# Kernel tuning notes

Hardware: AMD Instinct MI355X
Metric: run time of the kernel (lower is better)

## Reference

```python
import jax, jax.numpy as jnp
import numpy as np

N, E, G = 4096, 65536, 64
C_IN, PE_DIM, H, L, HEADS, C_OUT = 64, 24, 128, 2, 4, 10
HD = H // HEADS


def setup_inputs() -> dict:
    key = jax.random.key(0)
    ks = iter(jax.random.split(key, 64))

    def nrm(shape, scale=0.05):
        return jax.random.normal(next(ks), shape, jnp.float32) * scale

    inp = {}
    inp["x"] = jax.random.normal(next(ks), (N, C_IN), jnp.float32)
    inp["lap_pe"] = jax.random.normal(next(ks), (N, 8), jnp.float32)
    inp["rw_pe"] = jax.random.normal(next(ks), (N, 16), jnp.float32)
    inp["edge_index"] = jax.random.randint(next(ks), (2, E), 0, N)
    inp["batch"] = jnp.sort(jax.random.randint(next(ks), (N,), 0, G))
    inp["Wp"] = nrm((C_IN + PE_DIM, H)); inp["bp"] = jnp.zeros((H,), jnp.float32)
    inp["gin_W1"] = nrm((L, H, H)); inp["gin_b1"] = jnp.zeros((L, H), jnp.float32)
    inp["gin_W2"] = nrm((L, H, H)); inp["gin_b2"] = jnp.zeros((L, H), jnp.float32)
    inp["bn1_g"] = jnp.ones((L, H), jnp.float32); inp["bn1_b"] = jnp.zeros((L, H), jnp.float32)
    inp["bn2_g"] = jnp.ones((L, H), jnp.float32); inp["bn2_b"] = jnp.zeros((L, H), jnp.float32)
    inp["bn3_g"] = jnp.ones((L, H), jnp.float32); inp["bn3_b"] = jnp.zeros((L, H), jnp.float32)
    inp["attn_in_w"] = nrm((L, H, 3 * H)); inp["attn_in_b"] = jnp.zeros((L, 3 * H), jnp.float32)
    inp["attn_out_w"] = nrm((L, H, H)); inp["attn_out_b"] = jnp.zeros((L, H), jnp.float32)
    inp["mlp_W1"] = nrm((L, H, 2 * H)); inp["mlp_b1"] = jnp.zeros((L, 2 * H), jnp.float32)
    inp["mlp_W2"] = nrm((L, 2 * H, H)); inp["mlp_b2"] = jnp.zeros((L, H), jnp.float32)
    inp["Wr1"] = nrm((H, H)); inp["br1"] = jnp.zeros((H,), jnp.float32)
    inp["Wr2"] = nrm((H, H)); inp["br2"] = jnp.zeros((H,), jnp.float32)
    inp["Wc"] = nrm((H, C_OUT)); inp["bc"] = jnp.zeros((C_OUT,), jnp.float32)
    return inp


def _bn(x, g, b):
    # BatchNorm1d over node dim, training-mode batch statistics (biased var)
    m = jnp.mean(x, axis=0)
    v = jnp.var(x, axis=0)
    return (x - m) * jax.lax.rsqrt(v + 1e-5) * g + b


def reference(x, lap_pe, rw_pe, edge_index, batch, Wp, bp,
              gin_W1, gin_b1, gin_W2, gin_b2,
              bn1_g, bn1_b, bn2_g, bn2_b, bn3_g, bn3_b,
              attn_in_w, attn_in_b, attn_out_w, attn_out_b,
              mlp_W1, mlp_b1, mlp_W2, mlp_b2,
              Wr1, br1, Wr2, br2, Wc, bc):
    pe = jnp.concatenate([lap_pe, rw_pe], axis=-1)          # [N, 24]
    h = jnp.concatenate([x, pe], axis=-1) @ Wp + bp         # [N, H]
    src, dst = edge_index[0], edge_index[1]
    scale = 1.0 / np.sqrt(HD)
    for l in range(L):
        # --- local GINConv: (1+eps)*x_i + sum_{j->i} x_j, eps=0, then 2-layer MLP ---
        agg = jax.ops.segment_sum(h[src], dst, num_segments=N)
        g = h + agg
        g = jax.nn.relu(g @ gin_W1[l] + gin_b1[l]) @ gin_W2[l] + gin_b2[l]
        g = _bn(g + h, bn1_g[l], bn1_b[l])                  # residual + norm1
        # --- global MHA; batch is NOT forwarded to GPSConv, so all N nodes form one dense graph ---
        qkv = h @ attn_in_w[l] + attn_in_b[l]               # [N, 3H]
        q, k, v = jnp.split(qkv, 3, axis=-1)
        q = q.reshape(N, HEADS, HD).transpose(1, 0, 2)      # [Hh, N, d]
        k = k.reshape(N, HEADS, HD).transpose(1, 0, 2)
        v = v.reshape(N, HEADS, HD).transpose(1, 0, 2)
        a = jax.nn.softmax(jnp.einsum('hnd,hmd->hnm', q, k) * scale, axis=-1)
        o = jnp.einsum('hnm,hmd->hnd', a, v).transpose(1, 0, 2).reshape(N, H)
        o = o @ attn_out_w[l] + attn_out_b[l]
        o = _bn(o + h, bn2_g[l], bn2_b[l])                  # residual + norm2
        # --- combine + FFN (channels -> 2*channels -> channels) + norm3 ---
        out = g + o
        m = jax.nn.relu(out @ mlp_W1[l] + mlp_b1[l]) @ mlp_W2[l] + mlp_b2[l]
        out = _bn(out + m, bn3_g[l], bn3_b[l])
        h = jax.nn.relu(out)                                # outer F.relu in GraphGPS
    pooled = jax.ops.segment_sum(h, batch, num_segments=G)  # global_add_pool
    r = jax.nn.relu(pooled @ Wr1 + br1)
    r = jax.nn.relu(r @ Wr2 + br2)                          # dropout(0.5) disabled (eval)
    return r @ Wc + bc                                      # [G, C_OUT]
```

## Files before the change

kernel.cpp:

```cpp
#include <hip/hip_runtime.h>
#include <hip/hip_bf16.h>
#include <math.h>

#define NN 4096
#define HH 128
#define EE 65536
#define GG 64
#define KSPLIT 8
#define KLEN (NN / KSPLIT)
#define SMEM_BYTES 14336

typedef unsigned short u16;
typedef unsigned int u32;
typedef __bf16 bf16x8 __attribute__((ext_vector_type(8)));
typedef float f32x4 __attribute__((ext_vector_type(4)));

__device__ inline u16 f2b(float f) {
  u32 u = __float_as_uint(f);
  u += 0x7FFFu + ((u >> 16) & 1u);
  return (u16)(u >> 16);
}
__device__ inline u32 pkbf2(float a, float b) {
  __hip_bfloat162 h = __float22bfloat162_rn(float2{a, b});
  u32 u; __builtin_memcpy(&u, &h, 4); return u;
}

struct TDesc { const float* src; int Ks, K, M, off; };
struct TPack { TDesc d[13]; };

__global__ __launch_bounds__(256) void transcount_k(TPack P, u16* __restrict__ dst,
    const int* __restrict__ ei, int* cnt) {
  if (blockIdx.x >= 1344) {
    int e = (blockIdx.x - 1344)*256 + threadIdx.x;
    atomicAdd(&cnt[ei[EE + e]], 1);
    return;
  }
  int idx = blockIdx.x * 256 + threadIdx.x;
  for (int i = 0; i < 13; i++) {
    int sz = P.d[i].K * P.d[i].M;
    if (idx < sz) {
      int m = idx / P.d[i].K;
      int k = idx - m * P.d[i].K;
      float v = (k < P.d[i].Ks) ? P.d[i].src[(size_t)k * P.d[i].M + m] : 0.f;
      dst[P.d[i].off + idx] = f2b(v);
      return;
    }
    idx -= sz;
  }
}

__global__ __launch_bounds__(256) void scan_k(const int* __restrict__ cnt,
    int* __restrict__ rowptr, int* __restrict__ cursor) {
  __shared__ int tot[256];
  int t = threadIdx.x;
  int base = t * 16;
  int loc[16]; int s = 0;
  #pragma unroll
  for (int i = 0; i < 16; i++) { loc[i] = s; s += cnt[base + i]; }
  tot[t] = s;
  __syncthreads();
  for (int off = 1; off < 256; off <<= 1) {
    int v = (t >= off) ? tot[t - off] : 0;
    __syncthreads();
    tot[t] += v;
    __syncthreads();
  }
  int excl = (t == 0) ? 0 : tot[t - 1];
  #pragma unroll
  for (int i = 0; i < 16; i++) {
    int p = excl + loc[i];
    rowptr[base + i] = p; cursor[base + i] = p;
  }
  if (t == 255) rowptr[NN] = excl + s;
}

__global__ __launch_bounds__(256) void aggcsr_k(const int* __restrict__ rowptr,
    const int* __restrict__ elist, const float* __restrict__ h,
    float* __restrict__ agg) {
  int d = blockIdx.x*2 + (threadIdx.x >> 7);
  int c = threadIdx.x & 127;
  int beg = rowptr[d], end = rowptr[d + 1];
  float acc = 0.f;
  for (int j = beg; j < end; j++)
    acc += h[(size_t)elist[j]*HH + c];
  agg[(size_t)d*HH + c] = acc;
}

struct GArgs {
  const float *A, *A2, *A3;
  const u16* Bt;
  const float* bias;
  float* C;
  const float *res, *res2;
  float* stats;
  const float *sbase, *pg1, *pb1, *pg2, *pb2;
  const float *opart, *lpart;
  u16 *qb, *kb, *vt;
  int K, M;
};

template <int ASTAGE, int EPI, int RELU>
__device__ void mgemm_dev(const GArgs& a, int bx, int by, char* smem) {
  char* Ab = smem;
  char* Bb = smem + 4096;
  float* affs = (float*)(smem + 12288);
  const int tid = threadIdx.x;
  const int n0 = bx * 32, m0 = by * 64;
  const int w = tid >> 6, lane = tid & 63;
  const int g = lane >> 4, li = lane & 15;
  const int wr = w >> 1, wc = w & 1;
  const int K = a.K, M = a.M;

  if (ASTAGE == 2) {
    int plane = tid >> 7, cc = tid & 127;
    const float* st = a.sbase + plane*256;
    const float* gg = plane ? a.pg2 : a.pg1;
    const float* bb = plane ? a.pb2 : a.pb1;
    float mean = st[cc] * (1.f/NN);
    float var  = st[128+cc] * (1.f/NN) - mean*mean;
    float s = rsqrtf(var + 1e-5f) * gg[cc];
    affs[plane*256 + cc]       = s;
    affs[plane*256 + 128 + cc] = bb[cc] - mean*s;
    __syncthreads();
  }

  f32x4 acc0 = {0,0,0,0}, acc1 = {0,0,0,0};
  const int arow = tid >> 3, akseg = (tid & 7) * 8;
  const int bcol = tid >> 2, bkseg = (tid & 3) * 16;

  for (int k0 = 0; k0 < K; k0 += 64) {
    {
      float4 a0 = {0,0,0,0}, a1 = {0,0,0,0};
      if (ASTAGE == 4) {
        int n = n0 + arow;
        if (k0 == 0) {
          a0 = *(const float4*)&a.A[(size_t)n*64 + akseg];
          a1 = *(const float4*)&a.A[(size_t)n*64 + akseg + 4];
        } else {
          if (akseg == 0)       { a0 = *(const float4*)&a.A2[(size_t)n*8];
                                  a1 = *(const float4*)&a.A2[(size_t)n*8 + 4]; }
          else if (akseg == 8)  { a0 = *(const float4*)&a.A3[(size_t)n*16];
                                  a1 = *(const float4*)&a.A3[(size_t)n*16 + 4]; }
          else if (akseg == 16) { a0 = *(const float4*)&a.A3[(size_t)n*16 + 8];
                                  a1 = *(const float4*)&a.A3[(size_t)n*16 + 12]; }
        }
      } else if (ASTAGE == 3) {
        int n = n0 + arow, c = k0 + akseg;
        int head = c >> 5, d0 = c & 31;
        float4 o0 = {0,0,0,0}, o1 = {0,0,0,0}; float L = 0.f;
        #pragma unroll
        for (int s = 0; s < KSPLIT; s++) {
          const float* ob = a.opart + ((size_t)(s*4+head)*NN + n)*32 + d0;
          float4 x0 = *(const float4*)ob, x1 = *(const float4*)(ob + 4);
          o0.x += x0.x; o0.y += x0.y; o0.z += x0.z; o0.w += x0.w;
          o1.x += x1.x; o1.y += x1.y; o1.z += x1.z; o1.w += x1.w;
          L += a.lpart[(size_t)(s*4+head)*NN + n];
        }
        float inv = 1.f / L;
        a0 = make_float4(o0.x*inv, o0.y*inv, o0.z*inv, o0.w*inv);
        a1 = make_float4(o1.x*inv, o1.y*inv, o1.z*inv, o1.w*inv);
      } else {
        const float* ap = a.A + (size_t)(n0 + arow) * K + k0 + akseg;
        a0 = *(const float4*)ap; a1 = *(const float4*)(ap + 4);
        if (ASTAGE == 1) {
          const float* p2 = a.A2 + (size_t)(n0 + arow) * K + k0 + akseg;
          float4 c0 = *(const float4*)p2, c1 = *(const float4*)(p2 + 4);
          a0.x += c0.x; a0.y += c0.y; a0.z += c0.z; a0.w += c0.w;
          a1.x += c1.x; a1.y += c1.y; a1.z += c1.z; a1.w += c1.w;
        } else if (ASTAGE == 2) {
          const float* p2 = a.A2 + (size_t)(n0 + arow) * K + k0 + akseg;
          float4 c0 = *(const float4*)p2, c1 = *(const float4*)(p2 + 4);
          const float* af = affs + k0 + akseg;
          float4 s1a = *(const float4*)af,         s1b = *(const float4*)(af + 4);
          float4 t1a = *(const float4*)(af + 128), t1b = *(const float4*)(af + 132);
          float4 s2a = *(const float4*)(af + 256), s2b = *(const float4*)(af + 260);
          float4 t2a = *(const float4*)(af + 384), t2b = *(const float4*)(af + 388);
          a0.x = a0.x*s1a.x + t1a.x + c0.x*s2a.x + t2a.x;
          a0.y = a0.y*s1a.y + t1a.y + c0.y*s2a.y + t2a.y;
          a0.z = a0.z*s1a.z + t1a.z + c0.z*s2a.z + t2a.z;
          a0.w = a0.w*s1a.w + t1a.w + c0.w*s2a.w + t2a.w;
          a1.x = a1.x*s1b.x + t1b.x + c1.x*s2b.x + t2b.x;
          a1.y = a1.y*s1b.y + t1b.y + c1.y*s2b.y + t2b.y;
          a1.z = a1.z*s1b.z + t1b.z + c1.z*s2b.z + t2b.z;
          a1.w = a1.w*s1b.w + t1b.w + c1.w*s2b.w + t2b.w;
        }
      }
      u16 t8[8] = {f2b(a0.x), f2b(a0.y), f2b(a0.z), f2b(a0.w),
                   f2b(a1.x), f2b(a1.y), f2b(a1.z), f2b(a1.w)};
      *(uint4*)(Ab + ((arow*128 + akseg*2) ^ ((arow & 7) << 4))) = *(uint4*)t8;
    }
    {
      const u16* bp = a.Bt + (size_t)(m0 + bcol) * K + k0 + bkseg;
      uint4 b0 = *(const uint4*)bp;
      uint4 b1 = *(const uint4*)(bp + 8);
      int ba = bcol*128 + bkseg*2;
      int sw = (bcol & 7) << 4;
      *(uint4*)(Bb + (ba ^ sw)) = b0;
      *(uint4*)(Bb + ((ba + 16) ^ sw)) = b1;
    }
    __syncthreads();
    int row = wr*16 + li;
    int cAl = wc*32 + li, cBl = cAl + 16;
    #pragma unroll
    for (int ck = 0; ck < 2; ck++) {
      bf16x8 af = *(const bf16x8*)(Ab + ((row*128 + ck*64 + g*16) ^ ((row & 7) << 4)));
      bf16x8 bf0 = *(const bf16x8*)(Bb + ((cAl*128 + ck*64 + g*16) ^ ((cAl & 7) << 4)));
      bf16x8 bf1 = *(const bf16x8*)(Bb + ((cBl*128 + ck*64 + g*16) ^ ((cBl & 7) << 4)));
      acc0 = __builtin_amdgcn_mfma_f32_16x16x32_bf16(af, bf0, acc0, 0, 0, 0);
      acc1 = __builtin_amdgcn_mfma_f32_16x16x32_bf16(af, bf1, acc1, 0, 0, 0);
    }
    __syncthreads();
  }

  const int colA = m0 + wc*32 + li, colB = colA + 16;
  const int colAl = wc*32 + li, colBl = colAl + 16;
  const int rbase = n0 + wr*16 + 4*g;

  if (EPI == 0) {
    float b0 = a.bias[colA], b1 = a.bias[colB];
    #pragma unroll
    for (int r = 0; r < 4; r++) {
      float v0 = acc0[r] + b0, v1 = acc1[r] + b1;
      if (RELU) { v0 = fmaxf(v0, 0.f); v1 = fmaxf(v1, 0.f); }
      a.C[(size_t)(rbase + r) * M + colA] = v0;
      a.C[(size_t)(rbase + r) * M + colB] = v1;
    }
  } else if (EPI == 1 || EPI == 3) {
    float b0 = a.bias[colA], b1 = a.bias[colB];
    float sA1=0, tA1=0, sA2=0, tA2=0, sB1=0, tB1=0, sB2=0, tB2=0;
    if (EPI == 3) {
      auto mk = [&](int col, float& s1, float& t1, float& s2, float& t2) {
        float m1 = a.sbase[col]*(1.f/NN), v1 = a.sbase[128+col]*(1.f/NN) - m1*m1;
        s1 = rsqrtf(v1 + 1e-5f) * a.pg1[col]; t1 = a.pb1[col] - m1*s1;
        float m2 = a.sbase[256+col]*(1.f/NN), v2 = a.sbase[384+col]*(1.f/NN) - m2*m2;
        s2 = rsqrtf(v2 + 1e-5f) * a.pg2[col]; t2 = a.pb2[col] - m2*s2;
      };
      mk(colA, sA1, tA1, sA2, tA2);
      mk(colB, sB1, tB1, sB2, tB2);
    }
    float s0 = 0, q0 = 0, s1 = 0, q1 = 0;
    #pragma unroll
    for (int r = 0; r < 4; r++) {
      int rw2 = rbase + r;
      float v0, v1;
      if (EPI == 1) {
        v0 = acc0[r] + b0 + a.res[(size_t)rw2 * 128 + colA];
        v1 = acc1[r] + b1 + a.res[(size_t)rw2 * 128 + colB];
      } else {
        v0 = acc0[r] + b0 + a.res[(size_t)rw2*128 + colA]*sA1 + tA1
                          + a.res2[(size_t)rw2*128 + colA]*sA2 + tA2;
        v1 = acc1[r] + b1 + a.res[(size_t)rw2*128 + colB]*sB1 + tB1
                          + a.res2[(size_t)rw2*128 + colB]*sB2 + tB2;
      }
      a.C[(size_t)rw2 * M + colA] = v0;
      a.C[(size_t)rw2 * M + colB] = v1;
      s0 += v0; q0 += v0*v0; s1 += v1; q1 += v1*v1;
    }
    s0 += __shfl_xor(s0, 16); s0 += __shfl_xor(s0, 32);
    q0 += __shfl_xor(q0, 16); q0 += __shfl_xor(q0, 32);
    s1 += __shfl_xor(s1, 16); s1 += __shfl_xor(s1, 32);
    q1 += __shfl_xor(q1, 16); q1 += __shfl_xor(q1, 32);
    float* sred = (float*)smem;
    if (lane < 16) {
      sred[wr*64 + colAl] = s0;  sred[128 + wr*64 + colAl] = q0;
      sred[wr*64 + colBl] = s1;  sred[128 + wr*64 + colBl] = q1;
    }
    __syncthreads();
    if (tid < 128) {
      int c = tid & 63, isq = tid >> 6;
      float v = sred[isq*128 + c] + sred[isq*128 + 64 + c];
      atomicAdd(&a.stats[isq*128 + m0 + c], v);
    }
  } else {
    const float QS = 0.17677669529663687f * 1.4426950408889634f;
    auto doq = [&](int col, f32x4 acc, float bb) {
      if (col < 128) {
        int hd = col >> 5, d = col & 31;
        #pragma unroll
        for (int r = 0; r < 4; r++)
          a.qb[((size_t)hd*NN + rbase + r)*32 + d] = f2b((acc[r] + bb) * QS);
      } else if (col < 256) {
        int hd = (col - 128) >> 5, d = col & 31;
        #pragma unroll
        for (int r = 0; r < 4; r++)
          a.kb[((size_t)hd*NN + rbase + r)*32 + d] = f2b(acc[r] + bb);
      } else {
        #pragma unroll
        for (int r = 0; r < 4; r++)
          a.vt[(size_t)(col - 256)*NN + rbase + r] = f2b(acc[r] + bb);
      }
    };
    doq(colA, acc0, a.bias[colA]);
    doq(colB, acc1, a.bias[colB]);
  }
}

template <int AS, int EP, int RE>
__global__ __launch_bounds__(256) void k_gemm(GArgs a) {
  extern __shared__ char smem[];
  mgemm_dev<AS, EP, RE>(a, blockIdx.x, blockIdx.y, smem);
}

__global__ __launch_bounds__(256) void k_qkv_gin1(GArgs qa, GArgs ga) {
  extern __shared__ char smem[];
  int b = blockIdx.x;
  if (b < 768) mgemm_dev<0,4,0>(qa, b & 127, b >> 7, smem);
  else { b -= 768; mgemm_dev<1,0,1>(ga, b & 127, b >> 7, smem); }
}

__global__ __launch_bounds__(256) void k_gin2_ao(GArgs g2, GArgs ao) {
  extern __shared__ char smem[];
  int b = blockIdx.x;
  if (b < 256) mgemm_dev<0,1,0>(g2, b & 127, b >> 7, smem);
  else { b -= 256; mgemm_dev<3,1,0>(ao, b & 127, b >> 7, smem); }
}

__global__ __launch_bounds__(256) void k_scat_inp(const int* __restrict__ ei,
    int* cursor, int* __restrict__ elist, GArgs ia) {
  extern __shared__ char smem[];
  int b = blockIdx.x;
  if (b < 256) {
    int e = b*256 + threadIdx.x;
    int d = ei[EE + e];
    int p = atomicAdd(&cursor[d], 1);
    elist[p] = ei[e];
  } else {
    b -= 256;
    mgemm_dev<4,0,0>(ia, b & 127, b >> 7, smem);
  }
}

__global__ __launch_bounds__(256) void bn3_k(
    const float* __restrict__ out3, const float* __restrict__ stats,
    const float* __restrict__ gamma, const float* __restrict__ beta,
    float* __restrict__ h, const int* __restrict__ batch,
    float* __restrict__ pooled, int dopool) {
  int idx = blockIdx.x*256 + threadIdx.x;
  int c = idx & 127;
  float mean = stats[c] * (1.f/NN);
  float var  = stats[128+c] * (1.f/NN) - mean*mean;
  float rs = rsqrtf(var + 1e-5f);
  float r = fmaxf((out3[idx] - mean) * rs * gamma[c] + beta[c], 0.f);
  if (dopool) atomicAdd(&pooled[batch[idx >> 7]*HH + c], r);
  else        h[idx] = r;
}

__global__ __launch_bounds__(256) void mfma_attn_k(
    const u16* __restrict__ qb, const u16* __restrict__ kb,
    const u16* __restrict__ vt, float* __restrict__ opart,
    float* __restrict__ lpart) {
  __shared__ __align__(16) u16 kbuf[2][2048];
  __shared__ __align__(16) u16 vbuf[2][2048];
  __shared__ __align__(16) u16 pbuf[4][1024];

  const int tid = threadIdx.x;
  const int w = tid >> 6, lane = tid & 63;
  const int g = lane >> 4, li = lane & 15;
  const int head = blockIdx.z;
  const int q0 = blockIdx.y * 128 + w * 16;
  const int j0 = blockIdx.x * KLEN;

  const bf16x8 qfA = *reinterpret_cast<const bf16x8*>(
      qb + ((size_t)(head*NN) + q0 + li)*32 + g*8);
  const bf16x8 qfB = *reinterpret_cast<const bf16x8*>(
      qb + ((size_t)(head*NN) + q0 + 64 + li)*32 + g*8);

  const int vd = tid >> 3;
  const int vcs = (tid & 7) ^ (vd & 7);
  const u16* kpan = kb + (size_t)head*NN*32;
  const u16* vrow_g = vt + (size_t)(head*32 + vd)*NN;

  f32x4 oA0 = {0,0,0,0}, oA1 = {0,0,0,0};
  f32x4 oB0 = {0,0,0,0}, oB1 = {0,0,0,0};
  const f32x4 zz = {0,0,0,0};
  float lsA = 0.f, lsB = 0.f;
  char* pb = (char*)&pbuf[w][0];
  const int swz = (li & 7) << 4;

  {
    uint4 kv = *(const uint4*)(kpan + (size_t)j0*32 + tid*8);
    uint4 vv = *(const uint4*)(vrow_g + j0 + vcs*8);
    *((uint4*)kbuf[0] + tid) = kv;
    *((uint4*)vbuf[0] + tid) = vv;
  }
  __syncthreads();

  const int NSTEP = KLEN / 64;
  int cur = 0;
  for (int s = 0; s < NSTEP; s++) {
    int jt = j0 + s*64;
    bool pf = (s + 1 < NSTEP);
    uint4 kv = {0,0,0,0}, vv = {0,0,0,0};
    if (pf) {
      kv = *(const uint4*)(kpan + (size_t)(jt + 64)*32 + tid*8);
      vv = *(const uint4*)(vrow_g + jt + 64 + vcs*8);
    }
    #pragma unroll
    for (int qq = 0; qq < 2; qq++) {
      const bf16x8 qf = qq ? qfB : qfA;
      f32x4 st[4];
      __builtin_amdgcn_s_setprio(1);
      #pragma unroll
      for (int t = 0; t < 4; t++) {
        bf16x8 kf = *(const bf16x8*)&kbuf[cur][(t*16 + li)*32 + g*8];
        st[t] = __builtin_amdgcn_mfma_f32_16x16x32_bf16(kf, qf, zz, 0, 0, 0);
      }
      __builtin_amdgcn_s_setprio(0);
      float lloc = 0.f;
      #pragma unroll
      for (int t = 0; t < 4; t++) {
        float p0 = exp2f(st[t][0]), p1 = exp2f(st[t][1]);
        float p2 = exp2f(st[t][2]), p3 = exp2f(st[t][3]);
        lloc += p0 + p1 + p2 + p3;
        uint2 wv2;
        wv2.x = pkbf2(p0, p1);
        wv2.y = pkbf2(p2, p3);
        *(uint2*)(pb + ((li*128 + t*32 + g*8) ^ swz)) = wv2;
      }
      if (qq) lsB += lloc; else lsA += lloc;
      __builtin_amdgcn_s_setprio(1);
      #pragma unroll
      for (int c = 0; c < 2; c++) {
        bf16x8 pa = *(const bf16x8*)(pb + ((li*128 + c*64 + g*16) ^ swz));
        int vs = ((c*4 + g) ^ (li & 7)) << 4;
        bf16x8 vb0 = *(const bf16x8*)((char*)vbuf[cur] + li*128 + vs);
        bf16x8 vb1 = *(const bf16x8*)((char*)vbuf[cur] + (16 + li)*128 + vs);
        if (qq) {
          oB0 = __builtin_amdgcn_mfma_f32_16x16x32_bf16(pa, vb0, oB0, 0, 0, 0);
          oB1 = __builtin_amdgcn_mfma_f32_16x16x32_bf16(pa, vb1, oB1, 0, 0, 0);
        } else {
          oA0 = __builtin_amdgcn_mfma_f32_16x16x32_bf16(pa, vb0, oA0, 0, 0, 0);
          oA1 = __builtin_amdgcn_mfma_f32_16x16x32_bf16(pa, vb1, oA1, 0, 0, 0);
        }
      }
      __builtin_amdgcn_s_setprio(0);
    }
    if (pf) {
      *((uint4*)kbuf[cur ^ 1] + tid) = kv;
      *((uint4*)vbuf[cur ^ 1] + tid) = vv;
    }
    __syncthreads();
    cur ^= 1;
  }
  lsA += __shfl_xor(lsA, 16);
  lsA += __shfl_xor(lsA, 32);
  lsB += __shfl_xor(lsB, 16);
  lsB += __shfl_xor(lsB, 32);

  size_t b = (size_t)(blockIdx.x*4 + head)*NN + q0;
  size_t b2 = b + 64;
  #pragma unroll
  for (int r = 0; r < 4; r++) {
    size_t ob = (b + 4*g + r)*32;
    opart[ob + li]      = oA0[r];
    opart[ob + 16 + li] = oA1[r];
    size_t ob2 = (b2 + 4*g + r)*32;
    opart[ob2 + li]      = oB0[r];
    opart[ob2 + 16 + li] = oB1[r];
  }
  if (lane < 16) {
    lpart[b + lane]  = lsA;
    lpart[b2 + lane] = lsB;
  }
}

__global__ __launch_bounds__(128) void head_k(
    const float* __restrict__ pooled,
    const float* __restrict__ Wr1, const float* __restrict__ br1,
    const float* __restrict__ Wr2, const float* __restrict__ br2,
    const float* __restrict__ Wc, const float* __restrict__ bc,
    float* __restrict__ out) {
  __shared__ float bufa[128], bufb[128];
  int g = blockIdx.x, c = threadIdx.x;
  bufa[c] = pooled[g*HH + c];
  __syncthreads();
  float acc = br1[c];
  #pragma unroll 8
  for (int k = 0; k < 128; k++) acc += bufa[k] * Wr1[k*128 + c];
  bufb[c] = fmaxf(acc, 0.f);
  __syncthreads();
  acc = br2[c];
  #pragma unroll 8
  for (int k = 0; k < 128; k++) acc += bufb[k] * Wr2[k*128 + c];
  bufa[c] = fmaxf(acc, 0.f);
  __syncthreads();
  if (c < 10) {
    acc = bc[c];
    #pragma unroll 8
    for (int k = 0; k < 128; k++) acc += bufa[k] * Wc[k*10 + c];
    out[g*10 + c] = acc;
  }
}

extern "C" void kernel_launch(void* const* d_in, const int* in_sizes, int n_in,
                              void* d_out, int out_size, void* d_ws, size_t ws_size,
                              hipStream_t stream) {
  const float* x      = (const float*)d_in[0];
  const float* lap    = (const float*)d_in[1];
  const float* rw     = (const float*)d_in[2];
  const int*   ei     = (const int*)d_in[3];
  const int*   batch  = (const int*)d_in[4];
  const float* Wp     = (const float*)d_in[5];
  const float* bp     = (const float*)d_in[6];
  const float* gin_W1 = (const float*)d_in[7];
  const float* gin_b1 = (const float*)d_in[8];
  const float* gin_W2 = (const float*)d_in[9];
  const float* gin_b2 = (const float*)d_in[10];
  const float* bn1_g  = (const float*)d_in[11];
  const float* bn1_b  = (const float*)d_in[12];
  const float* bn2_g  = (const float*)d_in[13];
  const float* bn2_b  = (const float*)d_in[14];
  const float* bn3_g  = (const float*)d_in[15];
  const float* bn3_b  = (const float*)d_in[16];
  const float* ain_w  = (const float*)d_in[17];
  const float* ain_b  = (const float*)d_in[18];
  const float* aout_w = (const float*)d_in[19];
  const float* aout_b = (const float*)d_in[20];
  const float* mlp_W1 = (const float*)d_in[21];
  const float* mlp_b1 = (const float*)d_in[22];
  const float* mlp_W2 = (const float*)d_in[23];
  const float* mlp_b2 = (const float*)d_in[24];
  const float* Wr1    = (const float*)d_in[25];
  const float* br1    = (const float*)d_in[26];
  const float* Wr2    = (const float*)d_in[27];
  const float* br2    = (const float*)d_in[28];
  const float* Wc     = (const float*)d_in[29];
  const float* bc     = (const float*)d_in[30];
  float* out = (float*)d_out;

  float* w = (float*)d_ws;
  float* h      = w + 0;
  float* agg    = w + 524288;
  float* gtmp   = w + 1048576;
  float* pre1   = w + 1572864;
  float* pre2   = w + 2097152;
  float* mlph   = w + 2621440;
  float* out3   = w + 3670016;
  float* opart  = w + 4194304;
  float* lpart  = w + 8388608;
  float* stats  = w + 8519680;
  float* pooled = w + 8521216;
  int*   cnt    = (int*)(w + 8529408);
  int*   rowptr = (int*)(w + 8533504);
  int*   cursor = (int*)(w + 8537608);
  int*   elist  = (int*)(w + 8541704);
  u16*   wts    = (u16*)(w + 8607240);
  u16*   qb     = (u16*)(w + 8779272);
  u16*   kb     = (u16*)(w + 9041416);
  u16*   vt     = (u16*)(w + 9303560);

  u16* wpt = wts;
  u16 *qkvWt[2], *g1t[2], *g2t[2], *aot[2], *m1t[2], *m2t[2];
  {
    int off = 16384;
    for (int l = 0; l < 2; l++) {
      qkvWt[l] = wts + off; off += 384*128;
      g1t[l]   = wts + off; off += 128*128;
      g2t[l]   = wts + off; off += 128*128;
      aot[l]   = wts + off; off += 128*128;
      m1t[l]   = wts + off; off += 256*128;
      m2t[l]   = wts + off; off += 128*256;
    }
  }
  TPack tp;
  {
    int ti = 0, toff = 0;
    auto addm = [&](const float* s, int Ks, int Kd, int Md) {
      tp.d[ti].src = s; tp.d[ti].Ks = Ks; tp.d[ti].K = Kd; tp.d[ti].M = Md;
      tp.d[ti].off = toff; toff += Kd * Md; ti++;
    };
    addm(Wp, 88, 128, 128);
    for (int l = 0; l < 2; l++) {
      addm(ain_w + l*HH*384, 128, 128, 384);
      addm(gin_W1 + l*HH*HH, 128, 128, 128);
      addm(gin_W2 + l*HH*HH, 128, 128, 128);
      addm(aout_w + l*HH*HH, 128, 128, 128);
      addm(mlp_W1 + l*HH*256, 128, 128, 256);
      addm(mlp_W2 + l*256*HH, 256, 256, 128);
    }
  }

  auto GA = [&](const float* A, const float* A2, const float* A3, const u16* Bt,
                const float* bias, float* C, const float* res, const float* res2,
                float* st, const float* sb, const float* g1, const float* b1,
                const float* g2, const float* b2, const float* op, const float* lp,
                u16* q, u16* k, u16* v, int K, int M) {
    GArgs a; a.A=A; a.A2=A2; a.A3=A3; a.Bt=Bt; a.bias=bias; a.C=C; a.res=res;
    a.res2=res2; a.stats=st; a.sbase=sb; a.pg1=g1; a.pb1=b1; a.pg2=g2; a.pb2=b2;
    a.opart=op; a.lpart=lp; a.qb=q; a.kb=k; a.vt=v; a.K=K; a.M=M; return a;
  };

  hipMemsetAsync(stats, 0, 13824*sizeof(float), stream);
  transcount_k<<<1600, 256, 0, stream>>>(tp, wts, ei, cnt);
  scan_k<<<1, 256, 0, stream>>>(cnt, rowptr, cursor);
  k_scat_inp<<<512, 256, SMEM_BYTES, stream>>>(ei, cursor, elist,
      GA(x, lap, rw, wpt, bp, h, nullptr, nullptr, nullptr, nullptr,
         nullptr, nullptr, nullptr, nullptr, nullptr, nullptr,
         nullptr, nullptr, nullptr, 128, 128));

  for (int l = 0; l < 2; l++) {
    float* st1 = stats + l*768;
    float* st2 = st1 + 256;
    float* st3 = st1 + 512;

    aggcsr_k<<<NN/2, 256, 0, stream>>>(rowptr, elist, h, agg);

    k_qkv_gin1<<<1024, 256, SMEM_BYTES, stream>>>(
        GA(h, nullptr, nullptr, qkvWt[l], ain_b + l*384, nullptr, nullptr,
           nullptr, nullptr, nullptr, nullptr, nullptr, nullptr, nullptr,
           nullptr, nullptr, qb, kb, vt, 128, 384),
        GA(h, agg, nullptr, g1t[l], gin_b1 + l*HH, gtmp, nullptr, nullptr,
           nullptr, nullptr, nullptr, nullptr, nullptr, nullptr,
           nullptr, nullptr, nullptr, nullptr, nullptr, 128, 128));

    mfma_attn_k<<<dim3(KSPLIT, NN/128, 4), 256, 0, stream>>>(qb, kb, vt, opart, lpart);

    k_gin2_ao<<<512, 256, SMEM_BYTES, stream>>>(
        GA(gtmp, nullptr, nullptr, g2t[l], gin_b2 + l*HH, pre1, h, nullptr,
           st1, nullptr, nullptr, nullptr, nullptr, nullptr,
           nullptr, nullptr, nullptr, nullptr, nullptr, 128, 128),
        GA(nullptr, nullptr, nullptr, aot[l], aout_b + l*HH, pre2, h, nullptr,
           st2, nullptr, nullptr, nullptr, nullptr, nullptr,
           opart, lpart, nullptr, nullptr, nullptr, 128, 128));

    k_gemm<2,0,1><<<dim3(128,4), 256, SMEM_BYTES, stream>>>(
        GA(pre1, pre2, nullptr, m1t[l], mlp_b1 + l*256, mlph, nullptr, nullptr,
           nullptr, st1, bn1_g + l*HH, bn1_b + l*HH, bn2_g + l*HH, bn2_b + l*HH,
           nullptr, nullptr, nullptr, nullptr, nullptr, 128, 256));
    k_gemm<0,3,0><<<dim3(128,2), 256, SMEM_BYTES, stream>>>(
        GA(mlph, nullptr, nullptr, m2t[l], mlp_b2 + l*HH, out3, pre1, pre2,
           st3, st1, bn1_g + l*HH, bn1_b + l*HH, bn2_g + l*HH, bn2_b + l*HH,
           nullptr, nullptr, nullptr, nullptr, nullptr, 256, 128));
    bn3_k<<<NN*HH/256, 256, 0, stream>>>(out3, st3, bn3_g + l*HH, bn3_b + l*HH,
                                         h, batch, pooled, l == 1);
  }

  head_k<<<GG, 128, 0, stream>>>(pooled, Wr1, br1, Wr2, br2, Wc, bc, out);
}
```

Measured before the change: 194.5 us.

## Fuse neighbor aggregation into QKV launch, co-launch attention with GIN1, store partials in bf16

The CSR neighbor aggregation now runs as extra blocks of the QKV GEMM launch, and the split-K attention runs as blocks of the same launch as the first GIN GEMM. Each layer therefore issues one fewer kernel and independent work shares the GPU. Attention partial outputs are written as bf16 instead of fp32, which halves the write and read traffic for the partial-sum buffer but adds rounding error to the partial sums. The attention kernel now uses dynamic shared memory sized for both paths, so the GEMM blocks in that launch reserve more LDS, which may lower their occupancy.

```diff
diff --git a/kernel.cpp b/kernel.cpp
--- a/kernel.cpp
+++ b/kernel.cpp
@@ -8,7 +8,8 @@
 #define GG 64
 #define KSPLIT 8
 #define KLEN (NN / KSPLIT)
-#define SMEM_BYTES 14336
+#define SMEM_GEMM 14336
+#define SMEM_ATTN 24576
 
 typedef unsigned short u16;
 typedef unsigned int u32;
@@ -74,18 +75,6 @@
   if (t == 255) rowptr[NN] = excl + s;
 }
 
-__global__ __launch_bounds__(256) void aggcsr_k(const int* __restrict__ rowptr,
-    const int* __restrict__ elist, const float* __restrict__ h,
-    float* __restrict__ agg) {
-  int d = blockIdx.x*2 + (threadIdx.x >> 7);
-  int c = threadIdx.x & 127;
-  int beg = rowptr[d], end = rowptr[d + 1];
-  float acc = 0.f;
-  for (int j = beg; j < end; j++)
-    acc += h[(size_t)elist[j]*HH + c];
-  agg[(size_t)d*HH + c] = acc;
-}
-
 struct GArgs {
   const float *A, *A2, *A3;
   const u16* Bt;
@@ -94,7 +83,8 @@
   const float *res, *res2;
   float* stats;
   const float *sbase, *pg1, *pb1, *pg2, *pb2;
-  const float *opart, *lpart;
+  const u16 *opart;
+  const float *lpart;
   u16 *qb, *kb, *vt;
   int K, M;
 };
@@ -150,10 +140,16 @@
         float4 o0 = {0,0,0,0}, o1 = {0,0,0,0}; float L = 0.f;
         #pragma unroll
         for (int s = 0; s < KSPLIT; s++) {
-          const float* ob = a.opart + ((size_t)(s*4+head)*NN + n)*32 + d0;
-          float4 x0 = *(const float4*)ob, x1 = *(const float4*)(ob + 4);
-          o0.x += x0.x; o0.y += x0.y; o0.z += x0.z; o0.w += x0.w;
-          o1.x += x1.x; o1.y += x1.y; o1.z += x1.z; o1.w += x1.w;
+          const u16* ob = a.opart + ((size_t)(s*4+head)*NN + n)*32 + d0;
+          uint4 xx = *(const uint4*)ob;
+          o0.x += __uint_as_float(xx.x << 16);
+          o0.y += __uint_as_float(xx.x & 0xffff0000u);
+          o0.z += __uint_as_float(xx.y << 16);
+          o0.w += __uint_as_float(xx.y & 0xffff0000u);
+          o1.x += __uint_as_float(xx.z << 16);
+          o1.y += __uint_as_float(xx.z & 0xffff0000u);
+          o1.z += __uint_as_float(xx.w << 16);
+          o1.w += __uint_as_float(xx.w & 0xffff0000u);
           L += a.lpart[(size_t)(s*4+head)*NN + n];
         }
         float inv = 1.f / L;
@@ -295,70 +291,16 @@
   }
 }
 
-template <int AS, int EP, int RE>
-__global__ __launch_bounds__(256) void k_gemm(GArgs a) {
-  extern __shared__ char smem[];
-  mgemm_dev<AS, EP, RE>(a, blockIdx.x, blockIdx.y, smem);
-}
-
-__global__ __launch_bounds__(256) void k_qkv_gin1(GArgs qa, GArgs ga) {
-  extern __shared__ char smem[];
-  int b = blockIdx.x;
-  if (b < 768) mgemm_dev<0,4,0>(qa, b & 127, b >> 7, smem);
-  else { b -= 768; mgemm_dev<1,0,1>(ga, b & 127, b >> 7, smem); }
-}
-
-__global__ __launch_bounds__(256) void k_gin2_ao(GArgs g2, GArgs ao) {
-  extern __shared__ char smem[];
-  int b = blockIdx.x;
-  if (b < 256) mgemm_dev<0,1,0>(g2, b & 127, b >> 7, smem);
-  else { b -= 256; mgemm_dev<3,1,0>(ao, b & 127, b >> 7, smem); }
-}
-
-__global__ __launch_bounds__(256) void k_scat_inp(const int* __restrict__ ei,
-    int* cursor, int* __restrict__ elist, GArgs ia) {
-  extern __shared__ char smem[];
-  int b = blockIdx.x;
-  if (b < 256) {
-    int e = b*256 + threadIdx.x;
-    int d = ei[EE + e];
-    int p = atomicAdd(&cursor[d], 1);
-    elist[p] = ei[e];
-  } else {
-    b -= 256;
-    mgemm_dev<4,0,0>(ia, b & 127, b >> 7, smem);
-  }
-}
-
-__global__ __launch_bounds__(256) void bn3_k(
-    const float* __restrict__ out3, const float* __restrict__ stats,
-    const float* __restrict__ gamma, const float* __restrict__ beta,
-    float* __restrict__ h, const int* __restrict__ batch,
-    float* __restrict__ pooled, int dopool) {
-  int idx = blockIdx.x*256 + threadIdx.x;
-  int c = idx & 127;
-  float mean = stats[c] * (1.f/NN);
-  float var  = stats[128+c] * (1.f/NN) - mean*mean;
-  float rs = rsqrtf(var + 1e-5f);
-  float r = fmaxf((out3[idx] - mean) * rs * gamma[c] + beta[c], 0.f);
-  if (dopool) atomicAdd(&pooled[batch[idx >> 7]*HH + c], r);
-  else        h[idx] = r;
-}
-
-__global__ __launch_bounds__(256) void mfma_attn_k(
-    const u16* __restrict__ qb, const u16* __restrict__ kb,
-    const u16* __restrict__ vt, float* __restrict__ opart,
-    float* __restrict__ lpart) {
-  __shared__ __align__(16) u16 kbuf[2][2048];
-  __shared__ __align__(16) u16 vbuf[2][2048];
-  __shared__ __align__(16) u16 pbuf[4][1024];
-
+__device__ void attn_dev(const u16* __restrict__ qb, const u16* __restrict__ kb,
+    const u16* __restrict__ vt, u16* __restrict__ opart,
+    float* __restrict__ lpart, int split, int qblk, int head, char* smem) {
+  u16* kbuf = (u16*)smem;
+  u16* vbuf = (u16*)(smem + 8192);
   const int tid = threadIdx.x;
   const int w = tid >> 6, lane = tid & 63;
   const int g = lane >> 4, li = lane & 15;
-  const int head = blockIdx.z;
-  const int q0 = blockIdx.y * 128 + w * 16;
-  const int j0 = blockIdx.x * KLEN;
+  const int q0 = qblk * 128 + w * 16;
+  const int j0 = split * KLEN;
 
   const bf16x8 qfA = *reinterpret_cast<const bf16x8*>(
       qb + ((size_t)(head*NN) + q0 + li)*32 + g*8);
@@ -374,14 +316,14 @@
   f32x4 oB0 = {0,0,0,0}, oB1 = {0,0,0,0};
   const f32x4 zz = {0,0,0,0};
   float lsA = 0.f, lsB = 0.f;
-  char* pb = (char*)&pbuf[w][0];
+  char* pb = smem + 16384 + w*2048;
   const int swz = (li & 7) << 4;
 
   {
     uint4 kv = *(const uint4*)(kpan + (size_t)j0*32 + tid*8);
     uint4 vv = *(const uint4*)(vrow_g + j0 + vcs*8);
-    *((uint4*)kbuf[0] + tid) = kv;
-    *((uint4*)vbuf[0] + tid) = vv;
+    *((uint4*)kbuf + tid) = kv;
+    *((uint4*)vbuf + tid) = vv;
   }
   __syncthreads();
 
@@ -402,7 +344,7 @@
       __builtin_amdgcn_s_setprio(1);
       #pragma unroll
       for (int t = 0; t < 4; t++) {
-        bf16x8 kf = *(const bf16x8*)&kbuf[cur][(t*16 + li)*32 + g*8];
+        bf16x8 kf = *(const bf16x8*)&kbuf[cur*2048 + (t*16 + li)*32 + g*8];
         st[t] = __builtin_amdgcn_mfma_f32_16x16x32_bf16(kf, qf, zz, 0, 0, 0);
       }
       __builtin_amdgcn_s_setprio(0);
@@ -423,8 +365,8 @@
       for (int c = 0; c < 2; c++) {
         bf16x8 pa = *(const bf16x8*)(pb + ((li*128 + c*64 + g*16) ^ swz));
         int vs = ((c*4 + g) ^ (li & 7)) << 4;
-        bf16x8 vb0 = *(const bf16x8*)((char*)vbuf[cur] + li*128 + vs);
-        bf16x8 vb1 = *(const bf16x8*)((char*)vbuf[cur] + (16 + li)*128 + vs);
+        bf16x8 vb0 = *(const bf16x8*)((char*)(vbuf + cur*2048) + li*128 + vs);
+        bf16x8 vb1 = *(const bf16x8*)((char*)(vbuf + cur*2048) + (16 + li)*128 + vs);
         if (qq) {
           oB0 = __builtin_amdgcn_mfma_f32_16x16x32_bf16(pa, vb0, oB0, 0, 0, 0);
           oB1 = __builtin_amdgcn_mfma_f32_16x16x32_bf16(pa, vb1, oB1, 0, 0, 0);
@@ -436,8 +378,8 @@
       __builtin_amdgcn_s_setprio(0);
     }
     if (pf) {
-      *((uint4*)kbuf[cur ^ 1] + tid) = kv;
-      *((uint4*)vbuf[cur ^ 1] + tid) = vv;
+      *((uint4*)(kbuf + (cur ^ 1)*2048) + tid) = kv;
+      *((uint4*)(vbuf + (cur ^ 1)*2048) + tid) = vv;
     }
     __syncthreads();
     cur ^= 1;
@@ -447,21 +389,94 @@
   lsB += __shfl_xor(lsB, 16);
   lsB += __shfl_xor(lsB, 32);
 
-  size_t b = (size_t)(blockIdx.x*4 + head)*NN + q0;
+  size_t b = (size_t)(split*4 + head)*NN + q0;
   size_t b2 = b + 64;
   #pragma unroll
   for (int r = 0; r < 4; r++) {
     size_t ob = (b + 4*g + r)*32;
-    opart[ob + li]      = oA0[r];
-    opart[ob + 16 + li] = oA1[r];
+    opart[ob + li]      = f2b(oA0[r]);
+    opart[ob + 16 + li] = f2b(oA1[r]);
     size_t ob2 = (b2 + 4*g + r)*32;
-    opart[ob2 + li]      = oB0[r];
-    opart[ob2 + 16 + li] = oB1[r];
+    opart[ob2 + li]      = f2b(oB0[r]);
+    opart[ob2 + 16 + li] = f2b(oB1[r]);
   }
   if (lane < 16) {
     lpart[b + lane]  = lsA;
     lpart[b2 + lane] = lsB;
   }
+}
+
+template <int AS, int EP, int RE>
+__global__ __launch_bounds__(256) void k_gemm(GArgs a) {
+  extern __shared__ char smem[];
+  mgemm_dev<AS, EP, RE>(a, blockIdx.x, blockIdx.y, smem);
+}
+
+__global__ __launch_bounds__(256) void k_qkv_agg(GArgs qa,
+    const int* __restrict__ rowptr, const int* __restrict__ elist,
+    const float* __restrict__ h, float* __restrict__ agg) {
+  extern __shared__ char smem[];
+  int b = blockIdx.x;
+  if (b < 768) { mgemm_dev<0,4,0>(qa, b & 127, b >> 7, smem); return; }
+  b -= 768;
+  int c = threadIdx.x & 127, sub = threadIdx.x >> 7;
+  #pragma unroll
+  for (int i = 0; i < 4; i++) {
+    int d = b*8 + sub + i*2;
+    int beg = rowptr[d], end = rowptr[d + 1];
+    float acc = 0.f;
+    for (int j = beg; j < end; j++)
+      acc += h[(size_t)elist[j]*HH + c];
+    agg[(size_t)d*HH + c] = acc;
+  }
+}
+
+__global__ __launch_bounds__(256) void k_attn_gin1(
+    const u16* __restrict__ qb, const u16* __restrict__ kb,
+    const u16* __restrict__ vt, u16* __restrict__ opart,
+    float* __restrict__ lpart, GArgs ga) {
+  extern __shared__ char smem[];
+  int b = blockIdx.x;
+  if (b < 1024) { attn_dev(qb, kb, vt, opart, lpart, b & 7, (b >> 3) & 31, b >> 8, smem); return; }
+  b -= 1024;
+  mgemm_dev<1,0,1>(ga, b & 127, b >> 7, smem);
+}
+
+__global__ __launch_bounds__(256) void k_gin2_ao(GArgs g2, GArgs ao) {
+  extern __shared__ char smem[];
+  int b = blockIdx.x;
+  if (b < 256) mgemm_dev<0,1,0>(g2, b & 127, b >> 7, smem);
+  else { b -= 256; mgemm_dev<3,1,0>(ao, b & 127, b >> 7, smem); }
+}
+
+__global__ __launch_bounds__(256) void k_scat_inp(const int* __restrict__ ei,
+    int* cursor, int* __restrict__ elist, GArgs ia) {
+  extern __shared__ char smem[];
+  int b = blockIdx.x;
+  if (b < 256) {
+    int e = b*256 + threadIdx.x;
+    int d = ei[EE + e];
+    int p = atomicAdd(&cursor[d], 1);
+    elist[p] = ei[e];
+  } else {
+    b -= 256;
+    mgemm_dev<4,0,0>(ia, b & 127, b >> 7, smem);
+  }
+}
+
+__global__ __launch_bounds__(256) void bn3_k(
+    const float* __restrict__ out3, const float* __restrict__ stats,
+    const float* __restrict__ gamma, const float* __restrict__ beta,
+    float* __restrict__ h, const int* __restrict__ batch,
+    float* __restrict__ pooled, int dopool) {
+  int idx = blockIdx.x*256 + threadIdx.x;
+  int c = idx & 127;
+  float mean = stats[c] * (1.f/NN);
+  float var  = stats[128+c] * (1.f/NN) - mean*mean;
+  float rs = rsqrtf(var + 1e-5f);
+  float r = fmaxf((out3[idx] - mean) * rs * gamma[c] + beta[c], 0.f);
+  if (dopool) atomicAdd(&pooled[batch[idx >> 7]*HH + c], r);
+  else        h[idx] = r;
 }
 
 __global__ __launch_bounds__(128) void head_k(
@@ -536,7 +551,7 @@
   float* pre2   = w + 2097152;
   float* mlph   = w + 2621440;
   float* out3   = w + 3670016;
-  float* opart  = w + 4194304;
+  u16*   opart  = (u16*)(w + 4194304);
   float* lpart  = w + 8388608;
   float* stats  = w + 8519680;
   float* pooled = w + 8521216;
@@ -583,7 +598,7 @@
   auto GA = [&](const float* A, const float* A2, const float* A3, const u16* Bt,
                 const float* bias, float* C, const float* res, const float* res2,
                 float* st, const float* sb, const float* g1, const float* b1,
-                const float* g2, const float* b2, const float* op, const float* lp,
+                const float* g2, const float* b2, const u16* op, const float* lp,
                 u16* q, u16* k, u16* v, int K, int M) {
     GArgs a; a.A=A; a.A2=A2; a.A3=A3; a.Bt=Bt; a.bias=bias; a.C=C; a.res=res;
     a.res2=res2; a.stats=st; a.sbase=sb; a.pg1=g1; a.pb1=b1; a.pg2=g2; a.pb2=b2;
@@ -593,7 +608,7 @@
   hipMemsetAsync(stats, 0, 13824*sizeof(float), stream);
   transcount_k<<<1600, 256, 0, stream>>>(tp, wts, ei, cnt);
   scan_k<<<1, 256, 0, stream>>>(cnt, rowptr, cursor);
-  k_scat_inp<<<512, 256, SMEM_BYTES, stream>>>(ei, cursor, elist,
+  k_scat_inp<<<512, 256, SMEM_GEMM, stream>>>(ei, cursor, elist,
       GA(x, lap, rw, wpt, bp, h, nullptr, nullptr, nullptr, nullptr,
          nullptr, nullptr, nullptr, nullptr, nullptr, nullptr,
          nullptr, nullptr, nullptr, 128, 128));
@@ -603,19 +618,19 @@
     float* st2 = st1 + 256;
     float* st3 = st1 + 512;
 
-    aggcsr_k<<<NN/2, 256, 0, stream>>>(rowptr, elist, h, agg);
-
-    k_qkv_gin1<<<1024, 256, SMEM_BYTES, stream>>>(
+    k_qkv_agg<<<1280, 256, SMEM_GEMM, stream>>>(
         GA(h, nullptr, nullptr, qkvWt[l], ain_b + l*384, nullptr, nullptr,
            nullptr, nullptr, nullptr, nullptr, nullptr, nullptr, nullptr,
            nullptr, nullptr, qb, kb, vt, 128, 384),
+        rowptr, elist, h, agg);
+
+    k_attn_gin1<<<1280, 256, SMEM_ATTN, stream>>>(
+        qb, kb, vt, opart, lpart,
         GA(h, agg, nullptr, g1t[l], gin_b1 + l*HH, gtmp, nullptr, nullptr,
            nullptr, nullptr, nullptr, nullptr, nullptr, nullptr,
            nullptr, nullptr, nullptr, nullptr, nullptr, 128, 128));
 
-    mfma_attn_k<<<dim3(KSPLIT, NN/128, 4), 256, 0, stream>>>(qb, kb, vt, opart, lpart);
-
-    k_gin2_ao<<<512, 256, SMEM_BYTES, stream>>>(
+    k_gin2_ao<<<512, 256, SMEM_GEMM, stream>>>(
         GA(gtmp, nullptr, nullptr, g2t[l], gin_b2 + l*HH, pre1, h, nullptr,
            st1, nullptr, nullptr, nullptr, nullptr, nullptr,
            nullptr, nullptr, nullptr, nullptr, nullptr, 128, 128),
@@ -623,11 +638,11 @@
            st2, nullptr, nullptr, nullptr, nullptr, nullptr,
            opart, lpart, nullptr, nullptr, nullptr, 128, 128));
 
-    k_gemm<2,0,1><<<dim3(128,4), 256, SMEM_BYTES, stream>>>(
+    k_gemm<2,0,1><<<dim3(128,4), 256, SMEM_GEMM, stream>>>(
         GA(pre1, pre2, nullptr, m1t[l], mlp_b1 + l*256, mlph, nullptr, nullptr,
            nullptr, st1, bn1_g + l*HH, bn1_b + l*HH, bn2_g + l*HH, bn2_b + l*HH,
            nullptr, nullptr, nullptr, nullptr, nullptr, 128, 256));
-    k_gemm<0,3,0><<<dim3(128,2), 256, SMEM_BYTES, stream>>>(
+    k_gemm<0,3,0><<<dim3(128,2), 256, SMEM_GEMM, stream>>>(
         GA(mlph, nullptr, nullptr, m2t[l], mlp_b2 + l*HH, out3, pre1, pre2,
            st3, st1, bn1_g + l*HH, bn1_b + l*HH, bn2_g + l*HH, bn2_b + l*HH,
            nullptr, nullptr, nullptr, nullptr, nullptr, 256, 128));
```

After: 218.3 us (median of 2 runs). +12.2%, slower.
